# Kernel optimization log

Measured on AMD Instinct MI355X. Metric: run time of the kernel, lower is better.

The kernel has to match this reference:

```python
import jax, jax.numpy as jnp
import numpy as np

D, NH, HD = 256, 8, 32          # d_model, heads, head_dim
NPTS, NLAY, FF = 4, 6, 1024     # dec_n_points, decoder layers, ffn dim
BS, HS, WS = 4, 96, 96
N = HS * WS                     # flattened source tokens (single level)
NQ = 300                        # object queries
EPS = 1e-5


def setup_inputs() -> dict:
    key = jax.random.key(0)
    ks = iter(jax.random.split(key, 48))

    def nrm(shape, s=0.05):
        return (jax.random.normal(next(ks), shape) * s).astype(jnp.float32)

    inp = {
        "aps": jax.random.normal(next(ks), (BS, N, D), jnp.float32),
        "dvs": jax.random.normal(next(ks), (BS, N, D), jnp.float32),
        "query_embeds": jax.random.normal(next(ks), (NQ, 2 * D), jnp.float32),
        "valid_ratios": jnp.ones((BS, 2), jnp.float32),
        # fusion gating linears (stored as (in, out); y = x @ W + b)
        "aps_w1": nrm((D, D)), "aps_b1": jnp.zeros((D,), jnp.float32),
        "aps_w2": nrm((D, D)), "aps_b2": jnp.zeros((D,), jnp.float32),
        "dvs_w1": nrm((D, D)), "dvs_b1": jnp.zeros((D,), jnp.float32),
        "dvs_w2": nrm((D, D)), "dvs_b2": jnp.zeros((D,), jnp.float32),
        "ref_w": nrm((D, 2)), "ref_b": jnp.zeros((2,), jnp.float32),
        # per-decoder-layer params, stacked along leading NLAY axis
        "sa_qkv_w": nrm((NLAY, D, 3 * D)), "sa_qkv_b": jnp.zeros((NLAY, 3 * D), jnp.float32),
        "sa_out_w": nrm((NLAY, D, D)), "sa_out_b": jnp.zeros((NLAY, D), jnp.float32),
        "off_w": nrm((NLAY, D, NH * NPTS * 2), 0.01),
        "off_b": nrm((NLAY, NH * NPTS * 2), 2.0),
        "attn_w": nrm((NLAY, D, NH * NPTS)), "attn_b": jnp.zeros((NLAY, NH * NPTS), jnp.float32),
        "val_w": nrm((NLAY, D, D)), "val_b": jnp.zeros((NLAY, D), jnp.float32),
        "cout_w": nrm((NLAY, D, D)), "cout_b": jnp.zeros((NLAY, D), jnp.float32),
        "ln1_w": jnp.ones((NLAY, D), jnp.float32), "ln1_b": jnp.zeros((NLAY, D), jnp.float32),
        "ln2_w": jnp.ones((NLAY, D), jnp.float32), "ln2_b": jnp.zeros((NLAY, D), jnp.float32),
        "ln3_w": jnp.ones((NLAY, D), jnp.float32), "ln3_b": jnp.zeros((NLAY, D), jnp.float32),
        "ffn_w1": nrm((NLAY, D, FF)), "ffn_b1": jnp.zeros((NLAY, FF), jnp.float32),
        "ffn_w2": nrm((NLAY, FF, D)), "ffn_b2": jnp.zeros((NLAY, D), jnp.float32),
        "mask": jnp.zeros((BS, N), bool),
        "spatial_shapes": jnp.array([[HS, WS]], jnp.int32),
    }
    return inp


def _layer_norm(x, w, b):
    mu = jnp.mean(x, -1, keepdims=True)
    var = jnp.mean((x - mu) ** 2, -1, keepdims=True)
    return (x - mu) * jax.lax.rsqrt(var + EPS) * w + b


def _forward(aps, dvs, query_embeds, valid_ratios,
             aps_w1, aps_b1, aps_w2, aps_b2,
             dvs_w1, dvs_b1, dvs_w2, dvs_b2,
             ref_w, ref_b,
             sa_qkv_w, sa_qkv_b, sa_out_w, sa_out_b,
             off_w, off_b, attn_w, attn_b, val_w, val_b, cout_w, cout_b,
             ln1_w, ln1_b, ln2_w, ln2_b, ln3_w, ln3_b,
             ffn_w1, ffn_b1, ffn_w2, ffn_b2,
             mask, spatial_shapes):
    bs = aps.shape[0]
    inv_sqrt_d = np.float32(1.0 / np.sqrt(D))
    # ---- cross-modal gating. Original computes full (N,N) QK^T then sums the
    # last axis; sum_j q_i.k_j == q_i . (sum_j k_j), so we use the O(N*d) form.
    aps_gate = jnp.einsum('bnd,bd->bn', aps @ aps_w1 + aps_b1,
                          jnp.sum(aps @ aps_w2 + aps_b2, axis=1)) * inv_sqrt_d
    dvs_gate = jnp.einsum('bnd,bd->bn', dvs @ dvs_w1 + dvs_b1,
                          jnp.sum(dvs @ dvs_w2 + dvs_b2, axis=1)) * inv_sqrt_d
    gate = jax.nn.softmax(jnp.stack([aps_gate, dvs_gate], -1), -1)  # (bs,N,2)
    src = gate[..., :1] * aps + gate[..., 1:] * dvs

    qpos = jnp.broadcast_to(query_embeds[None, :, :D], (bs, NQ, D))
    out = jnp.broadcast_to(query_embeds[None, :, D:], (bs, NQ, D))
    ref_pts = jax.nn.sigmoid(qpos @ ref_w + ref_b)                 # (bs,NQ,2)

    Hs = spatial_shapes[0, 0]
    Ws = spatial_shapes[0, 1]
    # reference_points[:, :, None] * valid_ratios[:, None][:, None] -> (bs,NQ,1,2)
    rp_in = ref_pts[:, :, None, :] * valid_ratios[:, None, None, :]
    inv_sqrt_hd = np.float32(1.0 / np.sqrt(HD))

    for l in range(NLAY):
        # ---- self attention (q=k=tgt+query_pos, v=tgt)
        qk = out + qpos
        qh = (qk @ sa_qkv_w[l, :, :D] + sa_qkv_b[l, :D]).reshape(bs, NQ, NH, HD)
        kh = (qk @ sa_qkv_w[l, :, D:2 * D] + sa_qkv_b[l, D:2 * D]).reshape(bs, NQ, NH, HD)
        vh = (out @ sa_qkv_w[l, :, 2 * D:] + sa_qkv_b[l, 2 * D:]).reshape(bs, NQ, NH, HD)
        att = jax.nn.softmax(jnp.einsum('bqhd,bkhd->bhqk', qh, kh) * inv_sqrt_hd, -1)
        sa = jnp.einsum('bhqk,bkhd->bqhd', att, vh).reshape(bs, NQ, D) @ sa_out_w[l] + sa_out_b[l]
        out = _layer_norm(out + sa, ln2_w[l], ln2_b[l])

        # ---- MSDeformAttn cross attention (single level)
        q = out + qpos
        value = jnp.where(mask[:, :, None], 0.0, src @ val_w[l] + val_b[l])
        value = value.reshape(bs, -1, NH, HD).transpose(0, 2, 1, 3)   # (bs,NH,N,HD)
        offs = (q @ off_w[l] + off_b[l]).reshape(bs, NQ, NH, 1, NPTS, 2)
        aw = jax.nn.softmax((q @ attn_w[l] + attn_b[l]).reshape(bs, NQ, NH, NPTS), -1)
        normalizer = jnp.stack([Ws, Hs]).astype(q.dtype)              # [W, H]
        loc = (rp_in[:, :, None, :, None, :] + offs / normalizer)[:, :, :, 0]  # (bs,NQ,NH,NPTS,2)
        # bilinear sampling == grid_sample(align_corners=False, padding=zeros)
        x = loc[..., 0] * Ws - 0.5
        y = loc[..., 1] * Hs - 0.5
        x0 = jnp.floor(x); y0 = jnp.floor(y)
        wx1 = x - x0; wy1 = y - y0

        def corner(xi, yi, w):
            valid = (xi >= 0) & (xi <= Ws - 1) & (yi >= 0) & (yi <= Hs - 1)
            idx = (jnp.clip(yi, 0, Hs - 1) * Ws + jnp.clip(xi, 0, Ws - 1)).astype(jnp.int32)
            idx = idx.transpose(0, 2, 1, 3).reshape(bs, NH, NQ * NPTS, 1)
            v = jnp.take_along_axis(value, idx, axis=2)              # (bs,NH,NQ*NPTS,HD)
            v = v.reshape(bs, NH, NQ, NPTS, HD).transpose(0, 2, 1, 3, 4)
            return v * (w * valid)[..., None]

        samp = (corner(x0, y0, (1 - wx1) * (1 - wy1))
                + corner(x0 + 1, y0, wx1 * (1 - wy1))
                + corner(x0, y0 + 1, (1 - wx1) * wy1)
                + corner(x0 + 1, y0 + 1, wx1 * wy1))                 # (bs,NQ,NH,NPTS,HD)
        ca = jnp.einsum('bqhp,bqhpd->bqhd', aw, samp).reshape(bs, NQ, D) @ cout_w[l] + cout_b[l]
        out = _layer_norm(out + ca, ln1_w[l], ln1_b[l])

        # ---- FFN
        ff = jax.nn.relu(out @ ffn_w1[l] + ffn_b1[l]) @ ffn_w2[l] + ffn_b2[l]
        out = _layer_norm(out + ff, ln3_w[l], ln3_b[l])

    # return_intermediate_dec=False -> decoder returns (output, reference_points)
    return out, ref_pts, ref_pts


def reference(aps, dvs, query_embeds, valid_ratios,
              aps_w1, aps_b1, aps_w2, aps_b2,
              dvs_w1, dvs_b1, dvs_w2, dvs_b2,
              ref_w, ref_b,
              sa_qkv_w, sa_qkv_b, sa_out_w, sa_out_b,
              off_w, off_b, attn_w, attn_b, val_w, val_b, cout_w, cout_b,
              ln1_w, ln1_b, ln2_w, ln2_b, ln3_w, ln3_b,
              ffn_w1, ffn_b1, ffn_w2, ffn_b2,
              mask, spatial_shapes):
    return _forward(aps, dvs, query_embeds, valid_ratios,
                    aps_w1, aps_b1, aps_w2, aps_b2,
                    dvs_w1, dvs_b1, dvs_w2, dvs_b2,
                    ref_w, ref_b,
                    sa_qkv_w, sa_qkv_b, sa_out_w, sa_out_b,
                    off_w, off_b, attn_w, attn_b, val_w, val_b, cout_w, cout_b,
                    ln1_w, ln1_b, ln2_w, ln2_b, ln3_w, ln3_b,
                    ffn_w1, ffn_b1, ffn_w2, ffn_b2,
                    mask, spatial_shapes)
```

## Files before the change

### kernel.cpp

```cpp
#include <hip/hip_runtime.h>
#include <math.h>

#define D 256
#define NHD 8
#define HDIM 32
#define NPTS 4
#define NLAY 6
#define FFD 1024
#define BSZ 4
#define NSRC 9216
#define NQ 300
#define NROWS (BSZ*NQ)
#define NVROWS (BSZ*NSRC)
#define CCHK 256
#define VSTRIDE 1536
#define LNEPS 1e-5f

typedef __attribute__((ext_vector_type(8))) short short8v;
typedef __attribute__((ext_vector_type(4))) float f32x4;

__device__ __forceinline__ unsigned short f2bf(float f){
  unsigned u = __float_as_uint(f);
  unsigned r = (u + 0x7FFFu + ((u>>16)&1u)) >> 16;
  return (unsigned short)r;
}
__device__ __forceinline__ float bf2f(unsigned short u){
  return __uint_as_float(((unsigned)u)<<16);
}

__device__ __forceinline__ float wred_sum(float v){
#pragma unroll
  for(int o=32;o>=1;o>>=1) v += __shfl_xor(v,o,64);
  return v;
}
__device__ __forceinline__ float bred_sum(float v, float* s){
  v = wred_sum(v);
  int lane = threadIdx.x & 63, wid = threadIdx.x >> 6;
  if(lane==0) s[wid]=v;
  __syncthreads();
  float r = s[0]+s[1]+s[2]+s[3];
  __syncthreads();
  return r;
}

__global__ void colsum_partial(const float* __restrict__ aps, const float* __restrict__ dvs,
                               float* __restrict__ pA, float* __restrict__ pD){
  __shared__ float4 sA[4][64]; __shared__ float4 sD[4][64];
  int blk = blockIdx.x; int b = blk / CCHK; int c = blk % CCHK;
  int t = threadIdx.x; int cl = t & 63; int rg = t >> 6;
  const int rows = NSRC / CCHK;
  size_t base = ((size_t)b*NSRC + (size_t)c*rows)*D + cl*4;
  float4 sa = make_float4(0.f,0.f,0.f,0.f), sd = sa;
  for(int r=rg; r<rows; r+=4){
    float4 va = *(const float4*)(aps + base + (size_t)r*D);
    float4 vd = *(const float4*)(dvs + base + (size_t)r*D);
    sa.x+=va.x; sa.y+=va.y; sa.z+=va.z; sa.w+=va.w;
    sd.x+=vd.x; sd.y+=vd.y; sd.z+=vd.z; sd.w+=vd.w;
  }
  sA[rg][cl]=sa; sD[rg][cl]=sd;
  __syncthreads();
  if(t < 64){
    float4 r0=sA[0][t],r1=sA[1][t],r2=sA[2][t],r3=sA[3][t];
    float4 o; o.x=r0.x+r1.x+r2.x+r3.x; o.y=r0.y+r1.y+r2.y+r3.y;
    o.z=r0.z+r1.z+r2.z+r3.z; o.w=r0.w+r1.w+r2.w+r3.w;
    *(float4*)(pA + ((size_t)b*CCHK+c)*D + t*4) = o;
  } else if(t < 128){
    int u=t-64;
    float4 r0=sD[0][u],r1=sD[1][u],r2=sD[2][u],r3=sD[3][u];
    float4 o; o.x=r0.x+r1.x+r2.x+r3.x; o.y=r0.y+r1.y+r2.y+r3.y;
    o.z=r0.z+r1.z+r2.z+r3.z; o.w=r0.w+r1.w+r2.w+r3.w;
    *(float4*)(pD + ((size_t)b*CCHK+c)*D + u*4) = o;
  }
}

__global__ void gate_s2(const float* __restrict__ pA, const float* __restrict__ pD,
                        const float* __restrict__ w2a, const float* __restrict__ b2a,
                        const float* __restrict__ w2d, const float* __restrict__ b2d,
                        const float* __restrict__ b1a, const float* __restrict__ b1d,
                        float* __restrict__ s2, float* __restrict__ cAB){
  __shared__ float sums[D]; __shared__ float red[4];
  int blk = blockIdx.x; int b = blk>>1; int mod = blk&1;
  int t = threadIdx.x;
  const float* pX = mod? pD : pA;
  const float* w2 = mod? w2d : w2a;
  const float* b2 = mod? b2d : b2a;
  const float* b1 = mod? b1d : b1a;
  float s=0.f;
  for(int c=0;c<CCHK;++c) s += pX[((size_t)b*CCHK+c)*D+t];
  sums[t]=s; __syncthreads();
  float v=0.f;
  for(int i=0;i<D;++i) v += sums[i]*w2[(size_t)i*D+t];
  v += (float)NSRC * b2[t];
  s2[(size_t)blk*D + t] = v;
  float c = bred_sum(b1[t]*v, red);
  if(t==0) cAB[mod*BSZ + b] = c;
}

__global__ void gate_t(const float* __restrict__ w1a, const float* __restrict__ w1d,
                       const float* __restrict__ s2,
                       float* __restrict__ tA, float* __restrict__ tD){
  int gw = blockIdx.x*4 + (threadIdx.x>>6);
  int lane = threadIdx.x & 63;
  int i = gw & 255; int bm = gw >> 8;
  int mod = bm & 1, b = bm >> 1;
  const float* w1 = mod? w1d : w1a;
  const float* s2v = s2 + (size_t)bm*D;
  float4 wv = *(const float4*)(w1 + (size_t)i*D + lane*4);
  float4 sv = *(const float4*)(s2v + lane*4);
  float d = wv.x*sv.x + wv.y*sv.y + wv.z*sv.z + wv.w*sv.w;
  d = wred_sum(d);
  if(lane==0){
    if(mod) tD[b*D+i] = d; else tA[b*D+i] = d;
  }
}

__global__ void gate_src(const float* __restrict__ aps, const float* __restrict__ dvs,
                         const float* __restrict__ tA, const float* __restrict__ tD,
                         const float* __restrict__ cAB, unsigned short* __restrict__ srcb){
  int w = threadIdx.x >> 6, lane = threadIdx.x & 63;
  size_t row = (size_t)blockIdx.x*4 + w;
  int b = (int)(row / NSRC);
  const float4* ap = (const float4*)(aps + row*D);
  const float4* dp = (const float4*)(dvs + row*D);
  const float4* tap = (const float4*)(tA + (size_t)b*D);
  const float4* tdp = (const float4*)(tD + (size_t)b*D);
  float4 a = ap[lane], dd = dp[lane], ta = tap[lane], td = tdp[lane];
  float ga = a.x*ta.x + a.y*ta.y + a.z*ta.z + a.w*ta.w;
  float gd = dd.x*td.x + dd.y*td.y + dd.z*td.z + dd.w*td.w;
  ga = (wred_sum(ga) + cAB[b]) * 0.0625f;
  gd = (wred_sum(gd) + cAB[BSZ+b]) * 0.0625f;
  float m = fmaxf(ga,gd);
  float ea = expf(ga-m), ed = expf(gd-m);
  float inv = 1.f/(ea+ed);
  float wa = ea*inv, wd = ed*inv;
  ushort4 o;
  o.x = f2bf(wa*a.x + wd*dd.x); o.y = f2bf(wa*a.y + wd*dd.y);
  o.z = f2bf(wa*a.z + wd*dd.z); o.w = f2bf(wa*a.w + wd*dd.w);
  ((ushort4*)(srcb + row*D))[lane] = o;
}

__global__ void wconv_all(const float* __restrict__ valw, const float* __restrict__ saqkvw,
                          const float* __restrict__ saoutw, const float* __restrict__ coutw,
                          const float* __restrict__ ffw1, const float* __restrict__ ffw2,
                          unsigned short* __restrict__ valT, unsigned short* __restrict__ qkvT,
                          unsigned short* __restrict__ saoutT, unsigned short* __restrict__ coutT,
                          unsigned short* __restrict__ ff1T, unsigned short* __restrict__ ff2T){
  __shared__ float tile[32][33];
  int bid = blockIdx.x;
  const float* W; unsigned short* Bt; int K, N, rel;
  if(bid < 384)      { W=valw;   Bt=valT;   K=256;  N=256;  rel=bid; }
  else if(bid < 1536){ W=saqkvw; Bt=qkvT;   K=256;  N=768;  rel=bid-384; }
  else if(bid < 1920){ W=saoutw; Bt=saoutT; K=256;  N=256;  rel=bid-1536; }
  else if(bid < 2304){ W=coutw;  Bt=coutT;  K=256;  N=256;  rel=bid-1920; }
  else if(bid < 3840){ W=ffw1;   Bt=ff1T;   K=256;  N=1024; rel=bid-2304; }
  else               { W=ffw2;   Bt=ff2T;   K=1024; N=256;  rel=bid-3840; }
  int nk = K>>5, nn = N>>5, tpl = nk*nn;
  int l = rel/tpl, rem = rel%tpl;
  int tk = rem % nk, tn = rem / nk;
  int tx = threadIdx.x & 31, ty = threadIdx.x >> 5;
  const float* Wl = W + (size_t)l*K*N;
  unsigned short* Btl = Bt + (size_t)l*N*K;
#pragma unroll
  for(int i=0;i<4;++i)
    tile[ty+i*8][tx] = Wl[(size_t)(tk*32+ty+i*8)*N + tn*32+tx];
  __syncthreads();
#pragma unroll
  for(int i=0;i<4;++i)
    Btl[(size_t)(tn*32+ty+i*8)*K + tk*32+tx] = f2bf(tile[tx][ty+i*8]);
}

__global__ void init_out_ref(const float* __restrict__ qe, const float* __restrict__ refw,
                             const float* __restrict__ refb,
                             float* __restrict__ outb, unsigned short* __restrict__ out_bf,
                             unsigned short* __restrict__ outpos_bf,
                             float* __restrict__ refp, float* __restrict__ dout){
  __shared__ float red[4];
  int q = blockIdx.x, t = threadIdx.x;
  float pos = qe[(size_t)q*2*D + t];
  float tgt = qe[(size_t)q*2*D + D + t];
  unsigned short tb = f2bf(tgt), tpb = f2bf(tgt+pos);
  for(int b=0;b<BSZ;++b){
    outb[((size_t)b*NQ+q)*D + t] = tgt;
    out_bf[((size_t)b*NQ+q)*D + t] = tb;
    outpos_bf[((size_t)b*NQ+q)*D + t] = tpb;
  }
  float d0 = bred_sum(pos*refw[t*2+0], red);
  float d1 = bred_sum(pos*refw[t*2+1], red);
  if(t<2){
    float dot = (t==0? d0 : d1) + refb[t];
    float r = 1.f/(1.f+expf(-dot));
    refp[q*2+t] = r;
    const size_t o1 = (size_t)BSZ*NQ*D;
    const size_t o2 = o1 + (size_t)BSZ*NQ*2;
    for(int b=0;b<BSZ;++b){
      dout[o1 + (b*NQ+q)*2 + t] = r;
      dout[o2 + (b*NQ+q)*2 + t] = r;
    }
  }
}

__global__ __launch_bounds__(256) void gemmb(
    const unsigned short* __restrict__ A,
    const unsigned short* __restrict__ A2,
    int ncut,
    const unsigned short* __restrict__ Bt,
    const float* __restrict__ bias,
    float* __restrict__ Cf, unsigned short* __restrict__ Cb,
    int M, int K, int N, int relu){
  __shared__ unsigned short As[64][40];
  __shared__ unsigned short Bs[64][40];
  int n0 = blockIdx.x*64, m0 = blockIdx.y*64;
  const unsigned short* Asrc = (A2 && n0 >= ncut) ? A2 : A;
  int t = threadIdx.x, wave = t>>6, lane = t&63;
  int wm = (wave>>1)*32, wn = (wave&1)*32;
  int hi = lane>>4, lo = lane&15;
  int sr = t>>2, sc = (t&3)*8;
  f32x4 acc[2][2];
#pragma unroll
  for(int i=0;i<2;++i)
#pragma unroll
    for(int j=0;j<2;++j)
#pragma unroll
      for(int r=0;r<4;++r) acc[i][j][r]=0.f;
  for(int k0=0;k0<K;k0+=32){
    uint4 av = make_uint4(0,0,0,0);
    int arow = m0+sr;
    if(arow < M) av = *(const uint4*)(Asrc + (size_t)arow*K + k0 + sc);
    *(uint4*)&As[sr][sc] = av;
    *(uint4*)&Bs[sr][sc] = *(const uint4*)(Bt + (size_t)(n0+sr)*K + k0 + sc);
    __syncthreads();
    short8v a0 = *(short8v*)&As[wm+lo][hi*8];
    short8v a1 = *(short8v*)&As[wm+16+lo][hi*8];
    short8v b0 = *(short8v*)&Bs[wn+lo][hi*8];
    short8v b1 = *(short8v*)&Bs[wn+16+lo][hi*8];
    acc[0][0] = __builtin_amdgcn_mfma_f32_16x16x32_bf16(a0,b0,acc[0][0],0,0,0);
    acc[0][1] = __builtin_amdgcn_mfma_f32_16x16x32_bf16(a0,b1,acc[0][1],0,0,0);
    acc[1][0] = __builtin_amdgcn_mfma_f32_16x16x32_bf16(a1,b0,acc[1][0],0,0,0);
    acc[1][1] = __builtin_amdgcn_mfma_f32_16x16x32_bf16(a1,b1,acc[1][1],0,0,0);
    __syncthreads();
  }
#pragma unroll
  for(int mf=0;mf<2;++mf){
#pragma unroll
    for(int nf=0;nf<2;++nf){
      int col = n0 + wn + nf*16 + lo;
      float bv = bias[col];
#pragma unroll
      for(int r=0;r<4;++r){
        int row = m0 + wm + mf*16 + hi*4 + r;
        if(row < M){
          float v = acc[mf][nf][r] + bv;
          if(relu) v = fmaxf(v, 0.f);
          if(Cf) Cf[(size_t)row*N+col] = v;
          if(Cb) Cb[(size_t)row*N+col] = f2bf(v);
        }
      }
    }
  }
}

__global__ __launch_bounds__(256) void mfma_value6(
    const unsigned short* __restrict__ Abf,
    const unsigned short* __restrict__ Bt,
    const float* __restrict__ bias,
    const unsigned char* __restrict__ rowmask,
    unsigned short* __restrict__ C){
  __shared__ unsigned short As[128][40];
  __shared__ unsigned short Bs[128][40];
  int m0 = blockIdx.x*128, n0 = blockIdx.y*128;
  int t = threadIdx.x;
  int wave = t>>6, lane = t&63;
  int wm = (wave>>1)*64, wn = (wave&1)*64;
  f32x4 acc[4][4];
#pragma unroll
  for(int i=0;i<4;++i)
#pragma unroll
    for(int j=0;j<4;++j)
#pragma unroll
      for(int r=0;r<4;++r) acc[i][j][r]=0.f;

  int r0 = t>>2, c0 = (t&3)*8;
  int r1 = (t+256)>>2;
  for(int k0=0;k0<256;k0+=32){
    *(uint4*)&As[r0][c0] = *(const uint4*)(Abf + (size_t)(m0+r0)*256 + k0 + c0);
    *(uint4*)&As[r1][c0] = *(const uint4*)(Abf + (size_t)(m0+r1)*256 + k0 + c0);
    *(uint4*)&Bs[r0][c0] = *(const uint4*)(Bt  + (size_t)(n0+r0)*256 + k0 + c0);
    *(uint4*)&Bs[r1][c0] = *(const uint4*)(Bt  + (size_t)(n0+r1)*256 + k0 + c0);
    __syncthreads();
    short8v a[4], bb[4];
#pragma unroll
    for(int mf=0;mf<4;++mf) a[mf]  = *(short8v*)&As[wm+mf*16+(lane&15)][(lane>>4)*8];
#pragma unroll
    for(int nf=0;nf<4;++nf) bb[nf] = *(short8v*)&Bs[wn+nf*16+(lane&15)][(lane>>4)*8];
#pragma unroll
    for(int mf=0;mf<4;++mf)
#pragma unroll
      for(int nf=0;nf<4;++nf)
        acc[mf][nf] = __builtin_amdgcn_mfma_f32_16x16x32_bf16(a[mf], bb[nf], acc[mf][nf], 0,0,0);
    __syncthreads();
  }
#pragma unroll
  for(int mf=0;mf<4;++mf){
    int rbase = m0 + wm + mf*16 + (lane>>4)*4;
#pragma unroll
    for(int nf=0;nf<4;++nf){
      int col = n0 + wn + nf*16 + (lane&15);
      float bv = bias[col];
#pragma unroll
      for(int r=0;r<4;++r){
        int row = rbase + r;
        float v = acc[mf][nf][r] + bv;
        if(rowmask[row]) v = 0.f;
        C[(size_t)row*VSTRIDE + col] = f2bf(v);
      }
    }
  }
}

__global__ __launch_bounds__(256) void self_attn_mfma(
    const unsigned short* __restrict__ qkvh,
    unsigned short* __restrict__ sa){
  __shared__ unsigned short P[64][328];
  __shared__ unsigned short Vt[32][328];
  int blk = blockIdx.x;
  int qt = blk % 5; int bh = blk / 5; int h = bh % NHD; int b = bh / NHD;
  int t = threadIdx.x, wv = t>>6, lane = t&63;
  int hi = lane>>4, lo = lane&15;
  {
    int c = t & 31, rb = t >> 5;
    for(int r = rb; r < 320; r += 8){
      unsigned short v = 0;
      if(r < 300) v = qkvh[(size_t)(b*300+r)*768 + 512 + h*32 + c];
      Vt[c][r] = v;
    }
  }
  __syncthreads();
  int m0 = qt*64 + wv*16;
  int qr = m0 + lo; if(qr > 299) qr = 299;
  short8v aq = *(const short8v*)(qkvh + (size_t)(b*300+qr)*768 + h*32 + hi*8);
  f32x4 s[19];
#pragma unroll
  for(int nt=0; nt<19; ++nt){
    int kr = nt*16 + lo; if(kr > 299) kr = 299;
    short8v bk = *(const short8v*)(qkvh + (size_t)(b*300+kr)*768 + 256 + h*32 + hi*8);
    f32x4 z; z[0]=0.f; z[1]=0.f; z[2]=0.f; z[3]=0.f;
    s[nt] = __builtin_amdgcn_mfma_f32_16x16x32_bf16(aq, bk, z, 0,0,0);
  }
  const float kSc = 0.25506009837f;
  float inv[4];
#pragma unroll
  for(int ri=0; ri<4; ++ri){
    float m = -1e30f;
#pragma unroll
    for(int nt=0; nt<19; ++nt){
      if(nt*16+lo < 300) m = fmaxf(m, s[nt][ri]);
    }
#pragma unroll
    for(int o=8;o>=1;o>>=1) m = fmaxf(m, __shfl_xor(m,o,64));
    float sum = 0.f;
#pragma unroll
    for(int nt=0; nt<19; ++nt){
      float p = 0.f;
      if(nt*16+lo < 300) p = exp2f((s[nt][ri]-m)*kSc);
      sum += p;
      P[wv*16 + hi*4 + ri][nt*16 + lo] = f2bf(p);
    }
    P[wv*16 + hi*4 + ri][304 + lo] = 0;
#pragma unroll
    for(int o=8;o>=1;o>>=1) sum += __shfl_xor(sum,o,64);
    inv[ri] = 1.f/sum;
  }
  f32x4 o0, o1;
#pragma unroll
  for(int r=0;r<4;++r){ o0[r]=0.f; o1[r]=0.f; }
#pragma unroll
  for(int kt=0; kt<10; ++kt){
    short8v ap = *(short8v*)&P[wv*16 + lo][kt*32 + hi*8];
    short8v b0 = *(short8v*)&Vt[lo][kt*32 + hi*8];
    short8v b1 = *(short8v*)&Vt[16+lo][kt*32 + hi*8];
    o0 = __builtin_amdgcn_mfma_f32_16x16x32_bf16(ap, b0, o0, 0,0,0);
    o1 = __builtin_amdgcn_mfma_f32_16x16x32_bf16(ap, b1, o1, 0,0,0);
  }
#pragma unroll
  for(int ri=0; ri<4; ++ri){
    int r = m0 + hi*4 + ri;
    if(r < 300){
      size_t base = (size_t)(b*300+r)*256 + h*32;
      sa[base + lo]      = f2bf(o0[ri]*inv[ri]);
      sa[base + 16 + lo] = f2bf(o1[ri]*inv[ri]);
    }
  }
}

__global__ void residual_ln(const float* __restrict__ base, const float* __restrict__ delta,
                            const float* __restrict__ w, const float* __restrict__ bvec,
                            float* __restrict__ dstf, unsigned short* __restrict__ dstb,
                            unsigned short* __restrict__ dstp, const float* __restrict__ qe){
  __shared__ float red[4];
  size_t row = blockIdx.x; int t = threadIdx.x;
  float v = base[row*D+t] + delta[row*D+t];
  float mean = bred_sum(v, red) * (1.f/D);
  float c = v - mean;
  float var = bred_sum(c*c, red) * (1.f/D);
  float y = c * rsqrtf(var + LNEPS) * w[t] + bvec[t];
  dstf[row*D+t] = y;
  if(dstb) dstb[row*D+t] = f2bf(y);
  if(dstp){
    int q = (int)(row % NQ);
    dstp[row*D+t] = f2bf(y + qe[(size_t)q*2*D + t]);
  }
}

__global__ void deform_attn(const float* __restrict__ outb, const float* __restrict__ qe,
                            const float* __restrict__ offw, const float* __restrict__ offb,
                            const float* __restrict__ attnw, const float* __restrict__ attnb,
                            const unsigned short* __restrict__ value, const float* __restrict__ refp,
                            const float* __restrict__ vr, const int* __restrict__ sshape,
                            unsigned short* __restrict__ ca){
  __shared__ float qrow[D];
  __shared__ float part[96][2];
  __shared__ float proj[96];
  int row = blockIdx.x; int b = row / NQ; int q = row % NQ;
  int t = threadIdx.x;
  qrow[t] = outb[(size_t)row*D + t] + qe[(size_t)q*2*D + t];
  __syncthreads();
  if(t < 192){
    int col = t >> 1, half = t & 1;
    float acc = 0.f;
    if(col < 64){
      const float* W = offw;
      for(int k=half*128; k<half*128+128; ++k) acc += qrow[k]*W[(size_t)k*64 + col];
    } else {
      const float* W = attnw; int c = col-64;
      for(int k=half*128; k<half*128+128; ++k) acc += qrow[k]*W[(size_t)k*32 + c];
    }
    part[col][half] = acc;
  }
  __syncthreads();
  if(t < 96) proj[t] = part[t][0] + part[t][1] + (t<64 ? offb[t] : attnb[t-64]);
  __syncthreads();

  int h = t>>5, hd = t&31;
  float Hf = (float)sshape[0], Wf = (float)sshape[1];
  int Ws = sshape[1];
  float rx = refp[q*2+0] * vr[b*2+0];
  float ry = refp[q*2+1] * vr[b*2+1];
  const float* lg = &proj[64 + h*4];
  float m = fmaxf(fmaxf(lg[0],lg[1]),fmaxf(lg[2],lg[3]));
  float e[4]; float esum=0.f;
#pragma unroll
  for(int p=0;p<4;++p){ e[p]=expf(lg[p]-m); esum+=e[p]; }
  float einv = 1.f/esum;
  const float* ofr = &proj[h*8];
  const unsigned short* vbase = value + ((size_t)b*NSRC)*VSTRIDE + h*HDIM + hd;
  float acc = 0.f;
#pragma unroll
  for(int p=0;p<NPTS;++p){
    float lx = rx + ofr[p*2+0]/Wf;
    float ly = ry + ofr[p*2+1]/Hf;
    float x = lx*Wf - 0.5f, y = ly*Hf - 0.5f;
    float x0 = floorf(x), y0 = floorf(y);
    float wx = x-x0, wy = y-y0;
    float sample = 0.f;
#pragma unroll
    for(int cy=0;cy<2;++cy){
#pragma unroll
      for(int cx=0;cx<2;++cx){
        float xi = x0+cx, yi = y0+cy;
        float wgt = (cx? wx : 1.f-wx) * (cy? wy : 1.f-wy);
        bool valid = (xi>=0.f)&&(xi<=Wf-1.f)&&(yi>=0.f)&&(yi<=Hf-1.f);
        if(valid){
          int idx = (int)fminf(fmaxf(yi,0.f),Hf-1.f)*Ws + (int)fminf(fmaxf(xi,0.f),Wf-1.f);
          sample += wgt * bf2f(vbase[(size_t)idx*VSTRIDE]);
        }
      }
    }
    acc += (e[p]*einv) * sample;
  }
  ca[(size_t)row*D + h*HDIM + hd] = f2bf(acc);
}

extern "C" void kernel_launch(void* const* d_in, const int* in_sizes, int n_in,
                              void* d_out, int out_size, void* d_ws, size_t ws_size,
                              hipStream_t stream){
  const float* aps=(const float*)d_in[0];
  const float* dvs=(const float*)d_in[1];
  const float* qe =(const float*)d_in[2];
  const float* vr =(const float*)d_in[3];
  const float* aps_w1=(const float*)d_in[4]; const float* aps_b1=(const float*)d_in[5];
  const float* aps_w2=(const float*)d_in[6]; const float* aps_b2=(const float*)d_in[7];
  const float* dvs_w1=(const float*)d_in[8]; const float* dvs_b1=(const float*)d_in[9];
  const float* dvs_w2=(const float*)d_in[10]; const float* dvs_b2=(const float*)d_in[11];
  const float* ref_w=(const float*)d_in[12]; const float* ref_b=(const float*)d_in[13];
  const float* saqkvw=(const float*)d_in[14]; const float* saqkvb=(const float*)d_in[15];
  const float* saoutw=(const float*)d_in[16]; const float* saoutb=(const float*)d_in[17];
  const float* offw=(const float*)d_in[18]; const float* offb=(const float*)d_in[19];
  const float* attnw=(const float*)d_in[20]; const float* attnb=(const float*)d_in[21];
  const float* valw=(const float*)d_in[22]; const float* valb=(const float*)d_in[23];
  const float* coutw=(const float*)d_in[24]; const float* coutb=(const float*)d_in[25];
  const float* ln1w=(const float*)d_in[26]; const float* ln1b=(const float*)d_in[27];
  const float* ln2w=(const float*)d_in[28]; const float* ln2b=(const float*)d_in[29];
  const float* ln3w=(const float*)d_in[30]; const float* ln3b=(const float*)d_in[31];
  const float* ffw1=(const float*)d_in[32]; const float* ffb1=(const float*)d_in[33];
  const float* ffw2=(const float*)d_in[34]; const float* ffb2=(const float*)d_in[35];
  const unsigned char* mask=(const unsigned char*)d_in[36];
  const int* sshape=(const int*)d_in[37];
  float* out = (float*)d_out;

  char* wsb = (char*)d_ws;
  size_t o = 0;
  unsigned short* srcb   = (unsigned short*)(wsb+o); o += (size_t)NVROWS*D*2;
  unsigned short* valT   = (unsigned short*)(wsb+o); o += (size_t)NLAY*D*D*2;
  unsigned short* qkvT   = (unsigned short*)(wsb+o); o += (size_t)NLAY*3*D*D*2;
  unsigned short* saoutT = (unsigned short*)(wsb+o); o += (size_t)NLAY*D*D*2;
  unsigned short* coutT  = (unsigned short*)(wsb+o); o += (size_t)NLAY*D*D*2;
  unsigned short* ff1T   = (unsigned short*)(wsb+o); o += (size_t)NLAY*D*FFD*2;
  unsigned short* ff2T   = (unsigned short*)(wsb+o); o += (size_t)NLAY*FFD*D*2;
  unsigned short* value  = (unsigned short*)(wsb+o); o += (size_t)NVROWS*VSTRIDE*2;
  float* pA    = (float*)(wsb+o); o += (size_t)BSZ*CCHK*D*4;
  float* pD    = (float*)(wsb+o); o += (size_t)BSZ*CCHK*D*4;
  float* s2    = (float*)(wsb+o); o += 2*BSZ*D*4;
  float* tA    = (float*)(wsb+o); o += BSZ*D*4;
  float* tD    = (float*)(wsb+o); o += BSZ*D*4;
  float* cAB   = (float*)(wsb+o); o += 16*4;
  float* refp  = (float*)(wsb+o); o += NQ*2*4;
  float* outb  = (float*)(wsb+o); o += (size_t)NROWS*D*4;
  float* tmpb  = (float*)(wsb+o); o += (size_t)NROWS*D*4;
  unsigned short* out_bf    = (unsigned short*)(wsb+o); o += (size_t)NROWS*D*2;
  unsigned short* outpos_bf = (unsigned short*)(wsb+o); o += (size_t)NROWS*D*2;
  unsigned short* qkvh_bf   = (unsigned short*)(wsb+o); o += (size_t)NROWS*3*D*2;
  unsigned short* sa_bf     = (unsigned short*)(wsb+o); o += (size_t)NROWS*D*2;
  unsigned short* ca_bf     = (unsigned short*)(wsb+o); o += (size_t)NROWS*D*2;
  unsigned short* ffh_bf    = (unsigned short*)(wsb+o); o += (size_t)NROWS*FFD*2;

  colsum_partial<<<BSZ*CCHK,256,0,stream>>>(aps,dvs,pA,pD);
  gate_s2<<<2*BSZ,256,0,stream>>>(pA,pD,aps_w2,aps_b2,dvs_w2,dvs_b2,aps_b1,dvs_b1,s2,cAB);
  gate_t<<<512,256,0,stream>>>(aps_w1,dvs_w1,s2,tA,tD);
  gate_src<<<NVROWS/4,256,0,stream>>>(aps,dvs,tA,tD,cAB,srcb);
  wconv_all<<<5376,256,0,stream>>>(valw,saqkvw,saoutw,coutw,ffw1,ffw2,
                                   valT,qkvT,saoutT,coutT,ff1T,ff2T);
  init_out_ref<<<NQ,256,0,stream>>>(qe,ref_w,ref_b,outb,out_bf,outpos_bf,refp,out);
  mfma_value6<<<dim3(NVROWS/128, VSTRIDE/128),256,0,stream>>>(srcb, valT, valb, mask, value);

  dim3 gqkv(12,19), g256(4,19), gffu(16,19);

  for(int l=0;l<NLAY;++l){
    const unsigned short* qkvTl = qkvT + (size_t)l*3*D*D;
    const float* bqkv = saqkvb + (size_t)l*3*D;
    gemmb<<<gqkv,256,0,stream>>>(outpos_bf, out_bf, 512, qkvTl, bqkv,
                                 nullptr, qkvh_bf, NROWS, D, 3*D, 0);
    self_attn_mfma<<<BSZ*NHD*5,256,0,stream>>>(qkvh_bf, sa_bf);
    gemmb<<<g256,256,0,stream>>>(sa_bf, nullptr, 0, saoutT+(size_t)l*D*D, saoutb+(size_t)l*D,
                                 tmpb, nullptr, NROWS, D, D, 0);
    residual_ln<<<NROWS,256,0,stream>>>(outb,tmpb,ln2w+(size_t)l*D,ln2b+(size_t)l*D,
                                        outb,nullptr,nullptr,qe);

    deform_attn<<<NROWS,256,0,stream>>>(outb,qe,
                                        offw+(size_t)l*D*64, offb+(size_t)l*64,
                                        attnw+(size_t)l*D*32, attnb+(size_t)l*32,
                                        value + (size_t)l*D, refp, vr, sshape, ca_bf);
    gemmb<<<g256,256,0,stream>>>(ca_bf, nullptr, 0, coutT+(size_t)l*D*D, coutb+(size_t)l*D,
                                 tmpb, nullptr, NROWS, D, D, 0);
    residual_ln<<<NROWS,256,0,stream>>>(outb,tmpb,ln1w+(size_t)l*D,ln1b+(size_t)l*D,
                                        outb,out_bf,nullptr,qe);

    gemmb<<<gffu,256,0,stream>>>(out_bf, nullptr, 0, ff1T+(size_t)l*D*FFD, ffb1+(size_t)l*FFD,
                                 nullptr, ffh_bf, NROWS, D, FFD, 1);
    gemmb<<<g256,256,0,stream>>>(ffh_bf, nullptr, 0, ff2T+(size_t)l*FFD*D, ffb2+(size_t)l*D,
                                 tmpb, nullptr, NROWS, FFD, D, 0);
    if(l==NLAY-1)
      residual_ln<<<NROWS,256,0,stream>>>(outb,tmpb,ln3w+(size_t)l*D,ln3b+(size_t)l*D,
                                          out,nullptr,nullptr,qe);
    else
      residual_ln<<<NROWS,256,0,stream>>>(outb,tmpb,ln3w+(size_t)l*D,ln3b+(size_t)l*D,
                                          outb,out_bf,outpos_bf,qe);
  }
}
```

Measured before the change: 732.7 us.

## Use direct global-to-LDS loads in value GEMM and fuse LayerNorm into deform attention

The value-projection GEMM now stages A and B tiles with global_load_lds DMA instead of going through registers. Its LDS tiles drop the padding so the per-wave destinations are contiguous, and the grid is flattened so that adjacent blocks walk the N dimension and reuse the same A rows. Separately, the residual+LayerNorm after self-attention is folded into the deformable-attention kernel, removing one launch per layer and a round trip of the activation rows through memory. The unpadded LDS layout may add bank conflicts on the MFMA fragment reads, and correctness depends on the compiler waiting for the DMA loads before the barrier.

```diff
diff --git a/kernel.cpp b/kernel.cpp
--- a/kernel.cpp
+++ b/kernel.cpp
@@ -18,6 +18,10 @@
 
 typedef __attribute__((ext_vector_type(8))) short short8v;
 typedef __attribute__((ext_vector_type(4))) float f32x4;
+
+#define GLOAD_LDS(g, l) __builtin_amdgcn_global_load_lds( \
+    (const __attribute__((address_space(1))) void*)(g), \
+    (__attribute__((address_space(3))) void*)(l), 16, 0, 0)
 
 __device__ __forceinline__ unsigned short f2bf(float f){
   unsigned u = __float_as_uint(f);
@@ -265,9 +269,10 @@
     const float* __restrict__ bias,
     const unsigned char* __restrict__ rowmask,
     unsigned short* __restrict__ C){
-  __shared__ unsigned short As[128][40];
-  __shared__ unsigned short Bs[128][40];
-  int m0 = blockIdx.x*128, n0 = blockIdx.y*128;
+  __shared__ unsigned short As[128][32];
+  __shared__ unsigned short Bs[128][32];
+  int id = blockIdx.x;
+  int m0 = (id/12)*128, n0 = (id%12)*128;
   int t = threadIdx.x;
   int wave = t>>6, lane = t&63;
   int wm = (wave>>1)*64, wn = (wave&1)*64;
@@ -279,13 +284,18 @@
 #pragma unroll
       for(int r=0;r<4;++r) acc[i][j][r]=0.f;
 
-  int r0 = t>>2, c0 = (t&3)*8;
-  int r1 = (t+256)>>2;
+  const unsigned short* Ag = Abf + (size_t)(m0 + wave*32 + (lane>>2))*256 + (lane&3)*8;
+  const unsigned short* Bg = Bt  + (size_t)(n0 + wave*32 + (lane>>2))*256 + (lane&3)*8;
+  unsigned short* Al0 = &As[wave*32][0];
+  unsigned short* Al1 = &As[wave*32+16][0];
+  unsigned short* Bl0 = &Bs[wave*32][0];
+  unsigned short* Bl1 = &Bs[wave*32+16][0];
+
   for(int k0=0;k0<256;k0+=32){
-    *(uint4*)&As[r0][c0] = *(const uint4*)(Abf + (size_t)(m0+r0)*256 + k0 + c0);
-    *(uint4*)&As[r1][c0] = *(const uint4*)(Abf + (size_t)(m0+r1)*256 + k0 + c0);
-    *(uint4*)&Bs[r0][c0] = *(const uint4*)(Bt  + (size_t)(n0+r0)*256 + k0 + c0);
-    *(uint4*)&Bs[r1][c0] = *(const uint4*)(Bt  + (size_t)(n0+r1)*256 + k0 + c0);
+    GLOAD_LDS(Ag + k0,           Al0);
+    GLOAD_LDS(Ag + k0 + 16*256,  Al1);
+    GLOAD_LDS(Bg + k0,           Bl0);
+    GLOAD_LDS(Bg + k0 + 16*256,  Bl1);
     __syncthreads();
     short8v a[4], bb[4];
 #pragma unroll
@@ -411,18 +421,28 @@
   }
 }
 
-__global__ void deform_attn(const float* __restrict__ outb, const float* __restrict__ qe,
-                            const float* __restrict__ offw, const float* __restrict__ offb,
-                            const float* __restrict__ attnw, const float* __restrict__ attnb,
-                            const unsigned short* __restrict__ value, const float* __restrict__ refp,
-                            const float* __restrict__ vr, const int* __restrict__ sshape,
-                            unsigned short* __restrict__ ca){
+__global__ void deform_attn_ln(const float* __restrict__ base, const float* __restrict__ delta,
+                               const float* __restrict__ lnw, const float* __restrict__ lnb,
+                               float* __restrict__ outb,
+                               const float* __restrict__ qe,
+                               const float* __restrict__ offw, const float* __restrict__ offb,
+                               const float* __restrict__ attnw, const float* __restrict__ attnb,
+                               const unsigned short* __restrict__ value, const float* __restrict__ refp,
+                               const float* __restrict__ vr, const int* __restrict__ sshape,
+                               unsigned short* __restrict__ ca){
   __shared__ float qrow[D];
   __shared__ float part[96][2];
   __shared__ float proj[96];
+  __shared__ float red[4];
   int row = blockIdx.x; int b = row / NQ; int q = row % NQ;
   int t = threadIdx.x;
-  qrow[t] = outb[(size_t)row*D + t] + qe[(size_t)q*2*D + t];
+  float v = base[(size_t)row*D+t] + delta[(size_t)row*D+t];
+  float mean = bred_sum(v, red) * (1.f/D);
+  float c = v - mean;
+  float var = bred_sum(c*c, red) * (1.f/D);
+  float y = c * rsqrtf(var + LNEPS) * lnw[t] + lnb[t];
+  outb[(size_t)row*D+t] = y;
+  qrow[t] = y + qe[(size_t)q*2*D + t];
   __syncthreads();
   if(t < 192){
     int col = t >> 1, half = t & 1;
@@ -431,8 +451,8 @@
       const float* W = offw;
       for(int k=half*128; k<half*128+128; ++k) acc += qrow[k]*W[(size_t)k*64 + col];
     } else {
-      const float* W = attnw; int c = col-64;
-      for(int k=half*128; k<half*128+128; ++k) acc += qrow[k]*W[(size_t)k*32 + c];
+      const float* W = attnw; int cc = col-64;
+      for(int k=half*128; k<half*128+128; ++k) acc += qrow[k]*W[(size_t)k*32 + cc];
     }
     part[col][half] = acc;
   }
@@ -458,9 +478,9 @@
   for(int p=0;p<NPTS;++p){
     float lx = rx + ofr[p*2+0]/Wf;
     float ly = ry + ofr[p*2+1]/Hf;
-    float x = lx*Wf - 0.5f, y = ly*Hf - 0.5f;
-    float x0 = floorf(x), y0 = floorf(y);
-    float wx = x-x0, wy = y-y0;
+    float x = lx*Wf - 0.5f, y2 = ly*Hf - 0.5f;
+    float x0 = floorf(x), y0 = floorf(y2);
+    float wx = x-x0, wy = y2-y0;
     float sample = 0.f;
 #pragma unroll
     for(int cy=0;cy<2;++cy){
@@ -540,7 +560,7 @@
   wconv_all<<<5376,256,0,stream>>>(valw,saqkvw,saoutw,coutw,ffw1,ffw2,
                                    valT,qkvT,saoutT,coutT,ff1T,ff2T);
   init_out_ref<<<NQ,256,0,stream>>>(qe,ref_w,ref_b,outb,out_bf,outpos_bf,refp,out);
-  mfma_value6<<<dim3(NVROWS/128, VSTRIDE/128),256,0,stream>>>(srcb, valT, valb, mask, value);
+  mfma_value6<<<(NVROWS/128)*(VSTRIDE/128),256,0,stream>>>(srcb, valT, valb, mask, value);
 
   dim3 gqkv(12,19), g256(4,19), gffu(16,19);
 
@@ -552,13 +572,12 @@
     self_attn_mfma<<<BSZ*NHD*5,256,0,stream>>>(qkvh_bf, sa_bf);
     gemmb<<<g256,256,0,stream>>>(sa_bf, nullptr, 0, saoutT+(size_t)l*D*D, saoutb+(size_t)l*D,
                                  tmpb, nullptr, NROWS, D, D, 0);
-    residual_ln<<<NROWS,256,0,stream>>>(outb,tmpb,ln2w+(size_t)l*D,ln2b+(size_t)l*D,
-                                        outb,nullptr,nullptr,qe);
-
-    deform_attn<<<NROWS,256,0,stream>>>(outb,qe,
-                                        offw+(size_t)l*D*64, offb+(size_t)l*64,
-                                        attnw+(size_t)l*D*32, attnb+(size_t)l*32,
-                                        value + (size_t)l*D, refp, vr, sshape, ca_bf);
+
+    deform_attn_ln<<<NROWS,256,0,stream>>>(outb, tmpb, ln2w+(size_t)l*D, ln2b+(size_t)l*D,
+                                           outb, qe,
+                                           offw+(size_t)l*D*64, offb+(size_t)l*64,
+                                           attnw+(size_t)l*D*32, attnb+(size_t)l*32,
+                                           value + (size_t)l*D, refp, vr, sshape, ca_bf);
     gemmb<<<g256,256,0,stream>>>(ca_bf, nullptr, 0, coutT+(size_t)l*D*D, coutb+(size_t)l*D,
                                  tmpb, nullptr, NROWS, D, D, 0);
     residual_ln<<<NROWS,256,0,stream>>>(outb,tmpb,ln1w+(size_t)l*D,ln1b+(size_t)l*D,
```

New measurement: 722.9 us. No clear change (-1.3%).
